# Kernel tuning notes

Measured on AMD Instinct MI355X. Metric: run time of the kernel, lower is better.

## Reference

```python
import jax, jax.numpy as jnp
import numpy as np

N_EMBD = 768
N_HEAD = 12
HEAD_DIM = N_EMBD // N_HEAD
N_FREE = 3
NEG = jnp.float32(-1e30)


def _piece_masks():
    """Static 64x64 boolean reachability masks for each chess piece type.
    mask[q, k] = True means query square q may attend to key square k.
    Self-attention (q == k) is always allowed so no row is fully masked."""
    sq = np.arange(64)
    r, c = sq // 8, sq % 8
    dr = r[None, :] - r[:, None]  # row(k) - row(q)
    dc = c[None, :] - c[:, None]
    adr, adc = np.abs(dr), np.abs(dc)
    eye = np.eye(64, dtype=bool)
    knight = ((adr == 1) & (adc == 2)) | ((adr == 2) & (adc == 1))
    bishop = (adr == adc) & (adr != 0)
    rook = ((adr == 0) ^ (adc == 0))
    queen = bishop | rook
    king = np.maximum(adr, adc) == 1
    pawn = (dr == 1) & (adc <= 1)  # one step forward + diagonal captures
    return {k: v | eye for k, v in dict(knight=knight, bishop=bishop, rook=rook,
                                        queen=queen, king=king, pawn=pawn).items()}

_PM = _piece_masks()
# head layout: 2 knight, 2 bishop, 2 rook, 1 queen, 1 king, 1 pawn, 3 free
_PIECE_ORDER = ['knight', 'knight', 'bishop', 'bishop', 'rook', 'rook',
                'queen', 'king', 'pawn']
_PIECE_BIAS = jnp.asarray(
    np.stack([np.where(_PM[p], 0.0, -1e30) for p in _PIECE_ORDER]).astype(np.float32))


def _rmsnorm(x):
    eps = jnp.asarray(jnp.finfo(x.dtype).eps, x.dtype)
    return x * jax.lax.rsqrt(jnp.mean(jnp.square(x), axis=-1, keepdims=True) + eps)


def setup_inputs() -> dict:
    key = jax.random.key(0)
    ks = jax.random.split(key, 6)
    B = 1024
    x = jax.random.normal(ks[0], (B, 64, N_EMBD), dtype=jnp.float32)
    scale = 0.02
    Wq = jax.random.normal(ks[1], (N_EMBD, N_EMBD), dtype=jnp.float32) * scale
    Wk = jax.random.normal(ks[2], (N_EMBD, N_EMBD), dtype=jnp.float32) * scale
    Wv = jax.random.normal(ks[3], (N_EMBD, N_EMBD), dtype=jnp.float32) * scale
    Wo = jax.random.normal(ks[4], (N_EMBD, N_EMBD), dtype=jnp.float32) * scale
    free_logits = jax.random.normal(ks[5], (N_FREE, 64, 64), dtype=jnp.float32) * scale
    return {"x": x, "Wq": Wq, "Wk": Wk, "Wv": Wv, "Wo": Wo,
            "free_logits": free_logits}


def reference(x, Wq, Wk, Wv, Wo, free_logits):
    B, T, C = x.shape  # T == 64
    def proj(W):
        return (x @ W).reshape(B, T, N_HEAD, HEAD_DIM).transpose(0, 2, 1, 3)
    q, k, v = proj(Wq), proj(Wk), proj(Wv)  # (B, H, 64, hd)
    q, k = _rmsnorm(q), _rmsnorm(k)
    # attention bias: fixed piece masks for heads 0..8, learnable log-sigmoid for free heads
    free_bias = jnp.log(jax.nn.sigmoid(free_logits) + 1e-6)  # (3, 64, 64)
    bias = jnp.concatenate([_PIECE_BIAS, free_bias], axis=0)  # (12, 64, 64)
    scale = 1.0 / jnp.sqrt(jnp.asarray(HEAD_DIM, x.dtype))
    scores = jnp.einsum('bhqd,bhkd->bhqk', q, k) * scale + bias[None]
    attn = jax.nn.softmax(scores, axis=-1)
    y = jnp.einsum('bhqk,bhkd->bhqd', attn, v)
    y = y.transpose(0, 2, 1, 3).reshape(B, T, C)
    return y @ Wo
```

## Files before the change

kernel.cpp:

```cpp
#include <hip/hip_runtime.h>
#include <hip/hip_bf16.h>

typedef __attribute__((ext_vector_type(8))) __bf16 bf16x8;
typedef __attribute__((ext_vector_type(4))) float f32x4;
typedef __attribute__((ext_vector_type(8))) unsigned short u16x8;
typedef __attribute__((ext_vector_type(4))) unsigned int u32x4;

#define DEVI static __device__ __forceinline__

DEVI unsigned short f2bf(float f) {
  unsigned u = __builtin_bit_cast(unsigned, f);
  u += 0x7fffu + ((u >> 16) & 1u);
  return (unsigned short)(u >> 16);
}

DEVI bf16x8 ldbf8(const void* p) {
  return __builtin_bit_cast(bf16x8, *(const u16x8*)p);
}

DEVI void gload_lds16(const void* g, void* l) {
  __builtin_amdgcn_global_load_lds(
      (const __attribute__((address_space(1))) void*)g,
      (__attribute__((address_space(3))) void*)l, 16, 0, 0);
}

__global__ __launch_bounds__(256)
void prep_x_kernel(const float* __restrict__ x, unsigned short* __restrict__ xb) {
  size_t i = (size_t)(blockIdx.x * 256 + threadIdx.x) * 8;
  const float4* s = (const float4*)(x + i);
  float4 a = s[0], b = s[1];
  u16x8 o;
  o[0] = f2bf(a.x); o[1] = f2bf(a.y); o[2] = f2bf(a.z); o[3] = f2bf(a.w);
  o[4] = f2bf(b.x); o[5] = f2bf(b.y); o[6] = f2bf(b.z); o[7] = f2bf(b.w);
  *(u16x8*)(xb + i) = o;
}

__global__ __launch_bounds__(256)
void prep_w_kernel(const float* __restrict__ Wq, const float* __restrict__ Wk,
                   const float* __restrict__ Wv, const float* __restrict__ Wo,
                   const float* __restrict__ fl,
                   unsigned short* __restrict__ wqkv,
                   unsigned short* __restrict__ wo_t,
                   float* __restrict__ fb) {
  const int NQKV = 2304 * 768;
  const int NO = 768 * 768;
  int idx = blockIdx.x * 256 + threadIdx.x;
  if (idx < NQKV) {
    int n = idx / 768, kk = idx - n * 768;
    int sel = n / 768;
    int col = n - sel * 768;
    const float* W = (sel == 0) ? Wq : (sel == 1) ? Wk : Wv;
    wqkv[idx] = f2bf(W[kk * 768 + col]);
  } else if (idx < NQKV + NO) {
    int j = idx - NQKV;
    int n = j / 768, kk = j - n * 768;
    wo_t[j] = f2bf(Wo[kk * 768 + n]);
  } else if (idx < NQKV + NO + 3 * 64 * 64) {
    int j = idx - NQKV - NO;
    float v = fl[j];
    fb[j] = logf(1.0f / (1.0f + expf(-v)) + 1e-6f);
  }
}

template <int MODE>
__global__ __launch_bounds__(512, 2)
void gemm256_kernel(const unsigned short* __restrict__ A,
                    const unsigned short* __restrict__ Bt,
                    unsigned short* __restrict__ q_ws,
                    unsigned short* __restrict__ k_ws,
                    unsigned short* __restrict__ vt_ws,
                    float* __restrict__ out, int nbn, int cpx) {
  __shared__ __align__(16) char lds[131072];
  const int tid = threadIdx.x;
  const int lane = tid & 63, wv = tid >> 6;
  const int wm = wv >> 2, wn = wv & 3;
  const int fq = lane >> 4, fr = lane & 15;
  const int bid0 = blockIdx.x;
  const int bid = (bid0 & 7) * cpx + (bid0 >> 3);
  const int bn = bid % nbn, bm = bid / nbn;

  f32x4 acc[8][4];
#pragma unroll
  for (int i = 0; i < 8; ++i)
#pragma unroll
    for (int j = 0; j < 4; ++j)
#pragma unroll
      for (int e = 0; e < 4; ++e) acc[i][j][e] = 0.f;

  auto STAGE = [&](int kt, int buf) {
#pragma unroll
    for (int c = 0; c < 4; ++c) {
      int lin = c * 512 + tid;
      int row = lin >> 3;
      int cs = (lin & 7) ^ (row & 7);
      size_t srcA;
      if constexpr (MODE == 0) {
        srcA = ((size_t)(bm * 256 + row) * 768 + kt * 64 + cs * 8) * 2;
      } else {
        int m = bm * 256 + row;
        srcA = (((size_t)(m >> 6) * 12 + kt) * 4096 + (size_t)(m & 63) * 64 + cs * 8) * 2;
      }
      gload_lds16((const char*)A + srcA, lds + buf * 65536 + c * 8192 + wv * 1024);
      size_t srcB = ((size_t)(bn * 256 + row) * 768 + kt * 64 + cs * 8) * 2;
      gload_lds16((const char*)Bt + srcB, lds + buf * 65536 + 32768 + c * 8192 + wv * 1024);
    }
  };

  auto COMPUTE = [&](int buf) {
    const char* Ab = lds + buf * 65536;
    const char* Bb = lds + buf * 65536 + 32768;
#pragma unroll
    for (int kk = 0; kk < 2; ++kk) {
      int koff = ((kk * 4 + fq) ^ (fr & 7)) * 16;
      bf16x8 b4[4];
#pragma unroll
      for (int j = 0; j < 4; ++j)
        b4[j] = ldbf8(Bb + (wn * 64 + j * 16 + fr) * 128 + koff);
#pragma unroll
      for (int i = 0; i < 8; ++i) {
        bf16x8 a_ = ldbf8(Ab + (wm * 128 + i * 16 + fr) * 128 + koff);
#pragma unroll
        for (int j = 0; j < 4; ++j)
          acc[i][j] = __builtin_amdgcn_mfma_f32_16x16x32_bf16(a_, b4[j], acc[i][j], 0, 0, 0);
      }
    }
  };

  STAGE(0, 0);
  for (int t = 0; t < 11; ++t) {
    STAGE(t + 1, (t + 1) & 1);
    asm volatile("s_waitcnt vmcnt(8)" ::: "memory");
    asm volatile("s_barrier" ::: "memory");
    __builtin_amdgcn_s_setprio(1);
    COMPUTE(t & 1);
    __builtin_amdgcn_s_setprio(0);
    asm volatile("s_barrier" ::: "memory");
  }
  asm volatile("s_waitcnt vmcnt(0)" ::: "memory");
  asm volatile("s_barrier" ::: "memory");
  COMPUTE(1);

  if constexpr (MODE == 0) {
    const int ncb = bn * 256 + wn * 64;
    const int sector = ncb / 768;
    const int hh = (ncb % 768) >> 6;
#pragma unroll
    for (int i = 0; i < 8; ++i) {
      if (sector < 2) {
#pragma unroll
        for (int r = 0; r < 4; ++r) {
          float ss = 0.f;
#pragma unroll
          for (int j = 0; j < 4; ++j) { float v = acc[i][j][r]; ss += v * v; }
          ss += __shfl_xor(ss, 1);
          ss += __shfl_xor(ss, 2);
          ss += __shfl_xor(ss, 4);
          ss += __shfl_xor(ss, 8);
          float rms = rsqrtf(ss * 0.015625f + 1.1920929e-7f);
#pragma unroll
          for (int j = 0; j < 4; ++j) acc[i][j][r] *= rms;
        }
      }
#pragma unroll
      for (int r = 0; r < 4; ++r) {
        int m = bm * 256 + wm * 128 + i * 16 + fq * 4 + r;
        size_t base = (size_t)((m >> 6) * 12 + hh) * 4096;
        int t = m & 63;
#pragma unroll
        for (int j = 0; j < 4; ++j) {
          int d = j * 16 + fr;
          unsigned short v = f2bf(acc[i][j][r]);
          if (sector == 0) q_ws[base + t * 64 + d] = v;
          else if (sector == 1) k_ws[base + t * 64 + d] = v;
          else vt_ws[base + d * 64 + t] = v;
        }
      }
    }
  } else {
#pragma unroll
    for (int i = 0; i < 8; ++i)
#pragma unroll
      for (int r = 0; r < 4; ++r) {
        int m = bm * 256 + wm * 128 + i * 16 + fq * 4 + r;
        float* op = out + (size_t)m * 768 + bn * 256 + wn * 64 + fr;
#pragma unroll
        for (int j = 0; j < 4; ++j) op[j * 16] = acc[i][j][r];
      }
  }
}

DEVI float piece_bias(int h, int tq, int tk) {
  if (tq == tk) return 0.f;
  int rq = tq >> 3, cq = tq & 7;
  int rk = tk >> 3, ck = tk & 7;
  int dr = rk - rq, dc = ck - cq;
  int adr = dr < 0 ? -dr : dr, adc = dc < 0 ? -dc : dc;
  bool ok;
  if (h < 2)       ok = (adr == 1 && adc == 2) || (adr == 2 && adc == 1);
  else if (h < 4)  ok = (adr == adc);
  else if (h < 6)  ok = (adr == 0) != (adc == 0);
  else if (h == 6) ok = (adr == adc) || ((adr == 0) != (adc == 0));
  else if (h == 7) ok = (adr <= 1 && adc <= 1);
  else             ok = (dr == 1) && (adc <= 1);
  return ok ? 0.f : -1e30f;
}

__global__ __launch_bounds__(256, 4)
void attn_kernel(unsigned short* __restrict__ q_ws,
                 const unsigned short* __restrict__ k_ws,
                 const unsigned short* __restrict__ vt_ws,
                 const float* __restrict__ fb) {
  __shared__ __align__(16) unsigned short qs[4096];
  __shared__ __align__(16) unsigned short ks2[4096];
  __shared__ __align__(16) unsigned short vs[4096];
  __shared__ __align__(16) unsigned short ps[4096];
  const int bid = blockIdx.x;
  const int h = bid % 12;
  const int tid = threadIdx.x;
  const int lane = tid & 63, w = tid >> 6;
  const int fq = lane >> 4, fr = lane & 15;
  const size_t gb = (size_t)bid * 8192;

#pragma unroll
  for (int c = 0; c < 2; ++c) {
    int byte = (c * 256 + tid) * 16;
    int row = byte >> 7;
    int colb = byte & 127;
    int sw = (row << 7) | (colb ^ ((row & 7) << 4));
    u32x4 a = *(const u32x4*)((const char*)q_ws + gb + byte);
    u32x4 b = *(const u32x4*)((const char*)k_ws + gb + byte);
    u32x4 v = *(const u32x4*)((const char*)vt_ws + gb + byte);
    *(u32x4*)((char*)qs + sw) = a;
    *(u32x4*)((char*)ks2 + sw) = b;
    *(u32x4*)((char*)vs + sw) = v;
  }
  __syncthreads();

  f32x4 sacc[4];
#pragma unroll
  for (int j = 0; j < 4; ++j)
#pragma unroll
    for (int e = 0; e < 4; ++e) sacc[j][e] = 0.f;
#pragma unroll
  for (int kk = 0; kk < 2; ++kk) {
    int kbyte = kk * 64 + fq * 16;
    int rq = w * 16 + fr;
    bf16x8 af = ldbf8((const char*)qs + (rq << 7) + (kbyte ^ ((rq & 7) << 4)));
#pragma unroll
    for (int j = 0; j < 4; ++j) {
      int rk = j * 16 + fr;
      bf16x8 bf_ = ldbf8((const char*)ks2 + (rk << 7) + (kbyte ^ ((rk & 7) << 4)));
      sacc[j] = __builtin_amdgcn_mfma_f32_16x16x32_bf16(af, bf_, sacc[j], 0, 0, 0);
    }
  }

#pragma unroll
  for (int r = 0; r < 4; ++r) {
    int tq = w * 16 + fq * 4 + r;
    float s[4];
#pragma unroll
    for (int j = 0; j < 4; ++j) {
      int tk = j * 16 + fr;
      float bias = (h >= 9) ? fb[(h - 9) * 4096 + tq * 64 + tk] : piece_bias(h, tq, tk);
      s[j] = sacc[j][r] * 0.125f + bias;
    }
    float mx = fmaxf(fmaxf(s[0], s[1]), fmaxf(s[2], s[3]));
    mx = fmaxf(mx, __shfl_xor(mx, 1));
    mx = fmaxf(mx, __shfl_xor(mx, 2));
    mx = fmaxf(mx, __shfl_xor(mx, 4));
    mx = fmaxf(mx, __shfl_xor(mx, 8));
    float sum = 0.f;
#pragma unroll
    for (int j = 0; j < 4; ++j) { s[j] = __expf(s[j] - mx); sum += s[j]; }
    sum += __shfl_xor(sum, 1);
    sum += __shfl_xor(sum, 2);
    sum += __shfl_xor(sum, 4);
    sum += __shfl_xor(sum, 8);
    float inv = 1.f / sum;
#pragma unroll
    for (int j = 0; j < 4; ++j) {
      int tk = j * 16 + fr;
      *(unsigned short*)((char*)ps + (tq << 7) + ((tk * 2) ^ ((tq & 7) << 4))) =
          f2bf(s[j] * inv);
    }
  }
  __syncthreads();

  f32x4 yacc[4];
#pragma unroll
  for (int j = 0; j < 4; ++j)
#pragma unroll
    for (int e = 0; e < 4; ++e) yacc[j][e] = 0.f;
#pragma unroll
  for (int kk = 0; kk < 2; ++kk) {
    int kbyte = kk * 64 + fq * 16;
    int rp = w * 16 + fr;
    bf16x8 af = ldbf8((const char*)ps + (rp << 7) + (kbyte ^ ((rp & 7) << 4)));
#pragma unroll
    for (int j = 0; j < 4; ++j) {
      int rv = j * 16 + fr;
      bf16x8 bf_ = ldbf8((const char*)vs + (rv << 7) + (kbyte ^ ((rv & 7) << 4)));
      yacc[j] = __builtin_amdgcn_mfma_f32_16x16x32_bf16(af, bf_, yacc[j], 0, 0, 0);
    }
  }
#pragma unroll
  for (int r = 0; r < 4; ++r) {
    int tq = w * 16 + fq * 4 + r;
#pragma unroll
    for (int j = 0; j < 4; ++j) {
      int d = j * 16 + fr;
      q_ws[(size_t)bid * 4096 + tq * 64 + d] = f2bf(yacc[j][r]);
    }
  }
}

extern "C" void kernel_launch(void* const* d_in, const int* in_sizes, int n_in,
                              void* d_out, int out_size, void* d_ws, size_t ws_size,
                              hipStream_t stream) {
  const float* x  = (const float*)d_in[0];
  const float* Wq = (const float*)d_in[1];
  const float* Wk = (const float*)d_in[2];
  const float* Wv = (const float*)d_in[3];
  const float* Wo = (const float*)d_in[4];
  const float* fl = (const float*)d_in[5];
  float* out = (float*)d_out;

  char* ws = (char*)d_ws;
  unsigned short* wqkv = (unsigned short*)ws;
  unsigned short* wo_t = (unsigned short*)(ws + 3538944);
  float* fb = (float*)(ws + 3538944 + 1179648);
  char* big = ws + 3538944 + 1179648 + 49152;
  unsigned short* q_ws  = (unsigned short*)big;
  unsigned short* k_ws  = (unsigned short*)(big + 100663296ULL);
  unsigned short* vt_ws = (unsigned short*)(big + 201326592ULL);
  unsigned short* x_bf = (unsigned short*)d_out;

  prep_x_kernel<<<24576, 256, 0, stream>>>(x, x_bf);
  prep_w_kernel<<<9264, 256, 0, stream>>>(Wq, Wk, Wv, Wo, fl, wqkv, wo_t, fb);
  gemm256_kernel<0><<<2304, 512, 0, stream>>>(x_bf, wqkv, q_ws, k_ws, vt_ws, nullptr, 9, 288);
  attn_kernel<<<12288, 256, 0, stream>>>(q_ws, k_ws, vt_ws, fb);
  gemm256_kernel<1><<<768, 512, 0, stream>>>(q_ws, wo_t, nullptr, nullptr, nullptr, out, 3, 96);
}
```

Before: 899.7 us.

## Interleave LDS fragment loads, prefetch and MFMA in four-phase GEMM main loop

Restructures the GEMM K-loop so each tile is processed in four phases. Each phase loads a pair of A row fragments for both k-halves and runs MFMAs on them. B fragments are loaded once per tile, and the next tile's global-to-LDS prefetch is issued inside the first phase rather than before compute. The aim is finer-grained overlap of LDS reads, global loads and matrix ops. In exchange it adds many more barriers per tile and waits for all outstanding loads (vmcnt(0)) before the last phase.

```diff
diff --git a/kernel.cpp b/kernel.cpp
--- a/kernel.cpp
+++ b/kernel.cpp
@@ -106,39 +106,53 @@
     }
   };
 
-  auto COMPUTE = [&](int buf) {
-    const char* Ab = lds + buf * 65536;
-    const char* Bb = lds + buf * 65536 + 32768;
-#pragma unroll
-    for (int kk = 0; kk < 2; ++kk) {
-      int koff = ((kk * 4 + fq) ^ (fr & 7)) * 16;
-      bf16x8 b4[4];
-#pragma unroll
-      for (int j = 0; j < 4; ++j)
-        b4[j] = ldbf8(Bb + (wn * 64 + j * 16 + fr) * 128 + koff);
-#pragma unroll
-      for (int i = 0; i < 8; ++i) {
-        bf16x8 a_ = ldbf8(Ab + (wm * 128 + i * 16 + fr) * 128 + koff);
-#pragma unroll
-        for (int j = 0; j < 4; ++j)
-          acc[i][j] = __builtin_amdgcn_mfma_f32_16x16x32_bf16(a_, b4[j], acc[i][j], 0, 0, 0);
-      }
-    }
-  };
-
   STAGE(0, 0);
-  for (int t = 0; t < 11; ++t) {
-    STAGE(t + 1, (t + 1) & 1);
-    asm volatile("s_waitcnt vmcnt(8)" ::: "memory");
-    asm volatile("s_barrier" ::: "memory");
-    __builtin_amdgcn_s_setprio(1);
-    COMPUTE(t & 1);
-    __builtin_amdgcn_s_setprio(0);
-    asm volatile("s_barrier" ::: "memory");
-  }
   asm volatile("s_waitcnt vmcnt(0)" ::: "memory");
   asm volatile("s_barrier" ::: "memory");
-  COMPUTE(1);
+
+  const int koff0 = ((0 * 4 + fq) ^ (fr & 7)) * 16;
+  const int koff1 = ((1 * 4 + fq) ^ (fr & 7)) * 16;
+
+  for (int t = 0; t < 12; ++t) {
+    const char* Ab = lds + (t & 1) * 65536;
+    const char* Bb = Ab + 32768;
+    bf16x8 bfr[8];
+#pragma unroll
+    for (int q = 0; q < 4; ++q) {
+      int r0 = wm * 128 + (2 * q) * 16 + fr;
+      int r1 = r0 + 16;
+      bf16x8 a00 = ldbf8(Ab + r0 * 128 + koff0);
+      bf16x8 a01 = ldbf8(Ab + r0 * 128 + koff1);
+      bf16x8 a10 = ldbf8(Ab + r1 * 128 + koff0);
+      bf16x8 a11 = ldbf8(Ab + r1 * 128 + koff1);
+      if (q == 0) {
+#pragma unroll
+        for (int j = 0; j < 4; ++j) {
+          int rb = wn * 64 + j * 16 + fr;
+          bfr[j * 2 + 0] = ldbf8(Bb + rb * 128 + koff0);
+          bfr[j * 2 + 1] = ldbf8(Bb + rb * 128 + koff1);
+        }
+        if (t + 1 < 12) STAGE(t + 1, (t + 1) & 1);
+      }
+      if (q == 3) asm volatile("s_waitcnt vmcnt(0)" ::: "memory");
+      asm volatile("s_barrier" ::: "memory");
+      asm volatile("s_waitcnt lgkmcnt(0)" ::: "memory");
+      __builtin_amdgcn_s_setprio(1);
+#pragma unroll
+      for (int j = 0; j < 4; ++j) {
+        acc[2 * q][j] =
+            __builtin_amdgcn_mfma_f32_16x16x32_bf16(a00, bfr[j * 2 + 0], acc[2 * q][j], 0, 0, 0);
+        acc[2 * q][j] =
+            __builtin_amdgcn_mfma_f32_16x16x32_bf16(a01, bfr[j * 2 + 1], acc[2 * q][j], 0, 0, 0);
+        acc[2 * q + 1][j] =
+            __builtin_amdgcn_mfma_f32_16x16x32_bf16(a10, bfr[j * 2 + 0], acc[2 * q + 1][j], 0, 0, 0);
+        acc[2 * q + 1][j] =
+            __builtin_amdgcn_mfma_f32_16x16x32_bf16(a11, bfr[j * 2 + 1], acc[2 * q + 1][j], 0, 0, 0);
+      }
+      __builtin_amdgcn_s_setprio(0);
+      asm volatile("s_barrier" ::: "memory");
+    }
+  }
 
   if constexpr (MODE == 0) {
     const int ncb = bn * 256 + wn * 64;
```

Result: slower. 950.0 us (+5.6%).
